# Performance work log

Measured on AMD Instinct MI355X. Metric: run time of the kernel, lower is better.

## Reference

```python
import jax, jax.numpy as jnp
import numpy as np

N = 50000      # nodes
E = 1600000    # edges
IN = 128       # in_channels
H = 64         # hidden_channels
P = 200000     # edge pairs to score
BN_EPS = 1e-5


def setup_inputs() -> dict:
    key = jax.random.key(0)
    ks = jax.random.split(key, 24)
    lin = lambda k, i, o: jax.random.normal(k, (i, o), jnp.float32) / np.sqrt(i).astype(np.float32)
    return {
        "x": jax.random.normal(ks[0], (N, IN), jnp.float32),
        "edge_index": jax.random.randint(ks[1], (2, E), 0, N, jnp.int32),
        "src": jax.random.randint(ks[2], (P,), 0, N, jnp.int32),
        "dst": jax.random.randint(ks[3], (P,), 0, N, jnp.int32),
        # GCNConv weights/biases
        "W1": lin(ks[4], IN, H),        "b1": jnp.zeros((H,), jnp.float32),
        "W2": lin(ks[5], H, 2 * H),     "b2": jnp.zeros((2 * H,), jnp.float32),
        "W3": lin(ks[6], 2 * H, 2 * H), "b3": jnp.zeros((2 * H,), jnp.float32),
        # BatchNorm affine params
        "g1": jnp.ones((H,), jnp.float32),     "bt1": jnp.zeros((H,), jnp.float32),
        "g2": jnp.ones((2 * H,), jnp.float32), "bt2": jnp.zeros((2 * H,), jnp.float32),
        "g3": jnp.ones((2 * H,), jnp.float32), "bt3": jnp.zeros((2 * H,), jnp.float32),
        # edge-scoring MLP: Linear(4H -> 2H), ReLU, Linear(2H -> 1)
        "fcW1": lin(ks[7], 4 * H, 2 * H), "fcb1": jnp.zeros((2 * H,), jnp.float32),
        "fcW2": lin(ks[8], 2 * H, 1),     "fcb2": jnp.zeros((1,), jnp.float32),
    }


def _gcn_norm(edge_index):
    # add self-loops, symmetric normalization D^-1/2 (A+I) D^-1/2
    loop = jnp.arange(N, dtype=edge_index.dtype)
    row = jnp.concatenate([edge_index[0], loop])
    col = jnp.concatenate([edge_index[1], loop])
    deg = jax.ops.segment_sum(jnp.ones(row.shape, jnp.float32), col, num_segments=N)
    dis = jnp.where(deg > 0, jax.lax.rsqrt(deg), 0.0)
    norm = dis[row] * dis[col]
    return row, col, norm


def _conv(x, W, b, row, col, norm):
    h = x @ W                                  # [N, C]
    msg = h[row] * norm[:, None]               # [E+N, C] gather + scale
    agg = jax.ops.segment_sum(msg, col, num_segments=N)
    return agg + b


def _bn(x, g, bt):
    mu = x.mean(0)
    var = x.var(0)
    return g * (x - mu) * jax.lax.rsqrt(var + BN_EPS) + bt


def reference(x, edge_index, src, dst,
              W1, b1, W2, b2, W3, b3,
              g1, bt1, g2, bt2, g3, bt3,
              fcW1, fcb1, fcW2, fcb2):
    row, col, norm = _gcn_norm(edge_index)
    # inference path: dropout is identity; BN uses batch statistics
    z = _bn(jax.nn.relu(_conv(x, W1, b1, row, col, norm)), g1, bt1)
    z = _bn(jax.nn.relu(_conv(z, W2, b2, row, col, norm)), g2, bt2)
    z = _bn(jax.nn.relu(_conv(z, W3, b3, row, col, norm)), g3, bt3)
    # score(): gather-concat-MLP over edge pairs
    emb = jnp.concatenate([z[src], z[dst]], axis=1)   # [P, 4H]
    hidden = jax.nn.relu(emb @ fcW1 + fcb1)
    scores = (hidden @ fcW2 + fcb2).squeeze(-1)       # [P]
    return scores
```

## Files before the change

### kernel.cpp

```cpp
#include <hip/hip_runtime.h>
#include <math.h>

typedef short bf16x8 __attribute__((ext_vector_type(8)));
typedef float f32x4 __attribute__((ext_vector_type(4)));

#define BCAP 17408

__device__ inline unsigned int f2bf_pack(float lo, float hi) {
    unsigned int ul = __builtin_bit_cast(unsigned int, lo);
    unsigned int uh = __builtin_bit_cast(unsigned int, hi);
    ul = ul + 0x7fffu + ((ul >> 16) & 1u);
    uh = uh + 0x7fffu + ((uh >> 16) & 1u);
    return (ul >> 16) | (uh & 0xffff0000u);
}
__device__ inline unsigned short f2bf(float f) {
    unsigned int u = __builtin_bit_cast(unsigned int, f);
    u = u + 0x7fffu + ((u >> 16) & 1u);
    return (unsigned short)(u >> 16);
}
__device__ inline float bf2f(unsigned short u) {
    return __builtin_bit_cast(float, (unsigned int)u << 16);
}
__device__ inline float bflo(unsigned int w) { return __builtin_bit_cast(float, w << 16); }
__device__ inline float bfhi(unsigned int w) { return __builtin_bit_cast(float, w & 0xffff0000u); }


__global__ void k_seed(int* bcur, int NB) {
    int b = threadIdx.x;
    if (b < NB) bcur[b] = b * BCAP;
}

__global__ __launch_bounds__(256) void k_binA(const int* __restrict__ row, const int* __restrict__ col,
                                              int* __restrict__ bcur, int2* __restrict__ binned,
                                              int E, int NB) {
    constexpr int SLOTS = 32;
    constexpr int CHUNK = 2048;
    __shared__ int2 stage[128][SLOTS];
    __shared__ int lcount[128];
    for (int b = threadIdx.x; b < 128; b += 256) lcount[b] = 0;
    __syncthreads();
    for (int cs = blockIdx.x * CHUNK; cs < E; cs += gridDim.x * CHUNK) {
#pragma unroll
        for (int j = 0; j < CHUNK / 256; ++j) {
            int e = cs + j * 256 + threadIdx.x;
            if (e < E) {
                int r = row[e], c = col[e];
                int b = c >> 9;
                int pos = atomicAdd(&lcount[b], 1);
                if (pos < SLOTS) stage[b][pos] = make_int2(r, c);
                else {
                    int gp = atomicAdd(&bcur[b], 1);
                    binned[gp] = make_int2(r, c);
                }
            }
        }
        __syncthreads();
        for (int b = threadIdx.x; b < NB; b += 256) {
            int c = lcount[b];
            if (c > SLOTS) c = SLOTS;
            if (c > 0) {
                int gp = atomicAdd(&bcur[b], c);
                for (int j = 0; j < c; ++j) binned[gp + j] = stage[b][j];
            }
            lcount[b] = 0;
        }
        __syncthreads();
    }
}

__global__ void k_btop(const int* __restrict__ bcur, int* __restrict__ bstart,
                       int* __restrict__ offs, int NB, int N) {
    if (threadIdx.x == 0) {
        int acc = 0;
        for (int b = 0; b < NB; b++) {
            bstart[b] = acc;
            acc += bcur[b] - b * BCAP;
        }
        bstart[NB] = acc;
        offs[N] = acc;
    }
}

__global__ __launch_bounds__(1024) void k_binB1(const int2* __restrict__ binned, const int* __restrict__ bcur,
                                                const int* __restrict__ bstart, int* __restrict__ offs,
                                                float* __restrict__ dis, int N) {
    __shared__ int cnt[512];
    const int b = blockIdx.x;
    const int lo = b << 9;
    const int slab = b * BCAP;
    const int count = bcur[b] - slab;
    if (threadIdx.x < 512) cnt[threadIdx.x] = 0;
    __syncthreads();
    for (int i = threadIdx.x; i < count; i += 1024)
        atomicAdd(&cnt[binned[slab + i].y - lo], 1);
    __syncthreads();
    int own = 0;
    if (threadIdx.x < 512) own = cnt[threadIdx.x];
    for (int off = 1; off < 512; off <<= 1) {
        int t = 0;
        if (threadIdx.x < 512 && threadIdx.x >= off) t = cnt[threadIdx.x - off];
        __syncthreads();
        if (threadIdx.x < 512) cnt[threadIdx.x] += t;
        __syncthreads();
    }
    if (threadIdx.x < 512 && lo + threadIdx.x < N) {
        offs[lo + threadIdx.x] = bstart[b] + cnt[threadIdx.x] - own;
        dis[lo + threadIdx.x] = 1.0f / sqrtf((float)(own + 1));
    }
}

__global__ __launch_bounds__(1024) void k_binB2(const int2* __restrict__ binned, const int* __restrict__ bcur,
                                                const int* __restrict__ bstart, const int* __restrict__ offs,
                                                const float* __restrict__ dis, int2* __restrict__ csr, int N) {
    __shared__ int2 stage[BCAP];
    __shared__ int cur[512];
    const int b = blockIdx.x;
    const int lo = b << 9;
    const int slab = b * BCAP;
    const int count = bcur[b] - slab;
    const int base = bstart[b];
    if (threadIdx.x < 512) {
        int node = lo + threadIdx.x;
        cur[threadIdx.x] = (node < N ? offs[node] : base + count) - base;
    }
    __syncthreads();
    for (int i = threadIdx.x; i < count; i += 1024) {
        int2 e = binned[slab + i];
        int slot = atomicAdd(&cur[e.y - lo], 1);
        int2 o = make_int2(e.x, __builtin_bit_cast(int, dis[e.x]));
        if (slot < BCAP) stage[slot] = o;
        else csr[base + slot] = o;
    }
    __syncthreads();
    int lim = count < BCAP ? count : BCAP;
    for (int i = threadIdx.x; i < lim; i += 1024) csr[base + i] = stage[i];
}


__global__ __launch_bounds__(256) void k_cast(const float* __restrict__ X, unsigned short* __restrict__ Y, int n8) {
    int i = blockIdx.x * 256 + threadIdx.x;
    if (i >= n8) return;
    const float4* x4 = (const float4*)X;
    float4 a = x4[2 * i], b = x4[2 * i + 1];
    uint4 o = make_uint4(f2bf_pack(a.x, a.y), f2bf_pack(a.z, a.w),
                         f2bf_pack(b.x, b.y), f2bf_pack(b.z, b.w));
    *(uint4*)(Y + (size_t)i * 8) = o;
}


template <int K, int COUT>
__global__ __launch_bounds__(256) void k_prep(const float* __restrict__ W, unsigned short* __restrict__ Wt) {
    constexpr int NG = (COUT / 16) * (K / 32) * 64;
    int g = blockIdx.x * 256 + threadIdx.x;
    if (g >= NG) return;
    int l = g & 63;
    int ks = (g >> 6) % (K / 32);
    int nt = g / (64 * (K / 32));
    int n = nt * 16 + (l & 15);
    int k0 = ks * 32 + (l >> 4) * 8;
    unsigned int w[4];
#pragma unroll
    for (int j = 0; j < 4; ++j) {
        float a = W[(size_t)(k0 + 2 * j) * COUT + n];
        float b = W[(size_t)(k0 + 2 * j + 1) * COUT + n];
        w[j] = f2bf_pack(a, b);
    }
    *(uint4*)(Wt + (size_t)g * 8) = make_uint4(w[0], w[1], w[2], w[3]);
}


template <int K, int COUT, bool FUSED>
__global__ __launch_bounds__(256) void k_mgemm(const unsigned short* __restrict__ Xb,
                                               const unsigned short* __restrict__ Wt,
                                               const float* __restrict__ bias,
                                               unsigned short* __restrict__ H,
                                               float* __restrict__ part, int n) {
    constexpr int NT = COUT / 16;
    constexpr int KS = K / 32;
    __shared__ float reds[FUSED ? 16 : 1][COUT];
    __shared__ float redq[FUSED ? 16 : 1][COUT];
    const int lane = threadIdx.x & 63;
    const int wave = threadIdx.x >> 6;
    const int m = lane & 15, g4 = lane >> 4;
    const int rb = blockIdx.x * 64 + wave * 16;

    bf16x8 af[KS];
    {
        int arow = rb + m;
        if (arow >= n) arow = n - 1;
        const unsigned short* xr = Xb + (size_t)arow * K + g4 * 8;
#pragma unroll
        for (int ks = 0; ks < KS; ++ks) af[ks] = *(const bf16x8*)(xr + ks * 32);
    }
    const bf16x8* Wv = (const bf16x8*)Wt;
    f32x4 acc[NT];
#pragma unroll
    for (int nt = 0; nt < NT; ++nt) {
        f32x4 a = {0.f, 0.f, 0.f, 0.f};
#pragma unroll
        for (int ks = 0; ks < KS; ++ks)
            a = __builtin_amdgcn_mfma_f32_16x16x32_bf16(af[ks], Wv[(nt * KS + ks) * 64 + lane], a, 0, 0, 0);
        acc[nt] = a;
    }

    if (!FUSED) {
#pragma unroll
        for (int nt = 0; nt < NT; ++nt)
#pragma unroll
            for (int r = 0; r < 4; ++r) {
                int gr = rb + g4 * 4 + r;
                if (gr < n) H[(size_t)gr * COUT + nt * 16 + m] = f2bf(acc[nt][r]);
            }
    } else {
        float vs[NT], vq[NT];
#pragma unroll
        for (int nt = 0; nt < NT; ++nt) {
            float b1 = bias[nt * 16 + m];
            vs[nt] = 0.f; vq[nt] = 0.f;
#pragma unroll
            for (int r = 0; r < 4; ++r) {
                int gr = rb + g4 * 4 + r;
                bool ok = gr < n;
                float val = ok ? fmaxf(acc[nt][r] + b1, 0.f) : 0.f;
                if (ok) H[(size_t)gr * COUT + nt * 16 + m] = f2bf(val);
                vs[nt] += val;
                vq[nt] += val * val;
            }
        }
#pragma unroll
        for (int nt = 0; nt < NT; ++nt) {
            reds[wave * 4 + g4][nt * 16 + m] = vs[nt];
            redq[wave * 4 + g4][nt * 16 + m] = vq[nt];
        }
        __syncthreads();
        for (int c = threadIdx.x; c < COUT; c += 256) {
            float S = 0.f, Q = 0.f;
#pragma unroll
            for (int t = 0; t < 16; ++t) { S += reds[t][c]; Q += redq[t][c]; }
            part[(size_t)blockIdx.x * 2 * COUT + c] = S;
            part[(size_t)blockIdx.x * 2 * COUT + COUT + c] = Q;
        }
    }
}


__global__ __launch_bounds__(256) void k_agg64(const unsigned short* __restrict__ H, const int* __restrict__ offs,
                                               const int2* __restrict__ csr, const float* __restrict__ dis,
                                               const float* __restrict__ bias, unsigned short* __restrict__ Y,
                                               float* __restrict__ part, int n) {
    const int lane = threadIdx.x & 63;
    const int wave = threadIdx.x >> 6;
    const int gw = blockIdx.x * 4 + wave;
    const int nw = gridDim.x * 4;
    float bsum = 0.f, bsq = 0.f;
    const float bias_r = bias[lane];

    for (int node = gw; node < n; node += nw) {
        int s0 = offs[node], s1 = offs[node + 1];
        float a = 0.f;
        int e = s0;
        for (; e + 4 <= s1; e += 4) {
            int2 e0 = csr[e], e1 = csr[e + 1], e2 = csr[e + 2], e3 = csr[e + 3];
            float h0 = bf2f(H[(size_t)e0.x * 64 + lane]);
            float h1 = bf2f(H[(size_t)e1.x * 64 + lane]);
            float h2 = bf2f(H[(size_t)e2.x * 64 + lane]);
            float h3 = bf2f(H[(size_t)e3.x * 64 + lane]);
            a += __builtin_bit_cast(float, e0.y) * h0 + __builtin_bit_cast(float, e1.y) * h1;
            a += __builtin_bit_cast(float, e2.y) * h2 + __builtin_bit_cast(float, e3.y) * h3;
        }
        for (; e < s1; ++e) {
            int2 e0 = csr[e];
            a += __builtin_bit_cast(float, e0.y) * bf2f(H[(size_t)e0.x * 64 + lane]);
        }
        float dn = dis[node];
        float val = a * dn + bf2f(H[(size_t)node * 64 + lane]) * dn * dn + bias_r;
        val = fmaxf(val, 0.f);
        Y[(size_t)node * 64 + lane] = f2bf(val);
        bsum += val;
        bsq += val * val;
    }
    __shared__ float psum[4][64], psq[4][64];
    psum[wave][lane] = bsum; psq[wave][lane] = bsq;
    __syncthreads();
    if (threadIdx.x < 64) {
        int c = threadIdx.x;
        float s = psum[0][c] + psum[1][c] + psum[2][c] + psum[3][c];
        float qq = psq[0][c] + psq[1][c] + psq[2][c] + psq[3][c];
        part[(size_t)blockIdx.x * 128 + c] = s;
        part[(size_t)blockIdx.x * 128 + 64 + c] = qq;
    }
}


template <int C>
__global__ __launch_bounds__(256) void k_aggpre(const unsigned short* __restrict__ IN, const int* __restrict__ offs,
                                                const int2* __restrict__ csr, const float* __restrict__ dis,
                                                const float* __restrict__ ss, unsigned short* __restrict__ OUT, int n) {
    constexpr int VPL = C / 64;
    const int lane = threadIdx.x & 63;
    const int wave = threadIdx.x >> 6;
    const int gw = blockIdx.x * 4 + wave;
    const int nw = gridDim.x * 4;
    float sc[VPL], sh[VPL];
#pragma unroll
    for (int q = 0; q < VPL; q++) { sc[q] = ss[lane * VPL + q]; sh[q] = ss[C + lane * VPL + q]; }

    for (int node = gw; node < n; node += nw) {
        int s0 = offs[node], s1 = offs[node + 1];
        float a[VPL];
        float S = 0.f;
#pragma unroll
        for (int q = 0; q < VPL; q++) a[q] = 0.f;
        int e = s0;
        for (; e + 4 <= s1; e += 4) {
            int2 e0 = csr[e], e1 = csr[e + 1], e2 = csr[e + 2], e3 = csr[e + 3];
            float v0 = __builtin_bit_cast(float, e0.y);
            float v1 = __builtin_bit_cast(float, e1.y);
            float v2 = __builtin_bit_cast(float, e2.y);
            float v3 = __builtin_bit_cast(float, e3.y);
            S += (v0 + v1) + (v2 + v3);
            if (VPL == 2) {
                unsigned int w0 = *(const unsigned int*)(IN + (size_t)e0.x * C + 2 * lane);
                unsigned int w1 = *(const unsigned int*)(IN + (size_t)e1.x * C + 2 * lane);
                unsigned int w2 = *(const unsigned int*)(IN + (size_t)e2.x * C + 2 * lane);
                unsigned int w3 = *(const unsigned int*)(IN + (size_t)e3.x * C + 2 * lane);
                a[0] += v0 * bflo(w0) + v1 * bflo(w1) + v2 * bflo(w2) + v3 * bflo(w3);
                a[1] += v0 * bfhi(w0) + v1 * bfhi(w1) + v2 * bfhi(w2) + v3 * bfhi(w3);
            } else {
                float h0 = bf2f(IN[(size_t)e0.x * C + lane]);
                float h1 = bf2f(IN[(size_t)e1.x * C + lane]);
                float h2 = bf2f(IN[(size_t)e2.x * C + lane]);
                float h3 = bf2f(IN[(size_t)e3.x * C + lane]);
                a[0] += v0 * h0 + v1 * h1 + v2 * h2 + v3 * h3;
            }
        }
        for (; e < s1; ++e) {
            int2 e0 = csr[e];
            float v0 = __builtin_bit_cast(float, e0.y);
            S += v0;
            if (VPL == 2) {
                unsigned int w0 = *(const unsigned int*)(IN + (size_t)e0.x * C + 2 * lane);
                a[0] += v0 * bflo(w0);
                a[1] += v0 * bfhi(w0);
            } else {
                a[0] += v0 * bf2f(IN[(size_t)e0.x * C + lane]);
            }
        }
        float dn = dis[node];
        float shf = S + dn;
        if (VPL == 2) {
            unsigned int wsf = *(const unsigned int*)(IN + (size_t)node * C + 2 * lane);
            float o0 = dn * ((a[0] + dn * bflo(wsf)) * sc[0] + shf * sh[0]);
            float o1 = dn * ((a[1] + dn * bfhi(wsf)) * sc[1] + shf * sh[1]);
            *(unsigned int*)(OUT + (size_t)node * C + 2 * lane) = f2bf_pack(o0, o1);
        } else {
            float hsf = bf2f(IN[(size_t)node * C + lane]);
            OUT[(size_t)node * C + lane] = f2bf(dn * ((a[0] + dn * hsf) * sc[0] + shf * sh[0]));
        }
    }
}


template <int C>
__global__ __launch_bounds__(1024) void k_bnfin(const float* __restrict__ part, int nblk,
                                                const float* __restrict__ g, const float* __restrict__ bt,
                                                float* __restrict__ ss, int n) {
    constexpr int ROWS = 1024 / C;
    __shared__ float ssum[1024], ssq[1024];
    const int c = threadIdx.x % C;
    const int r = threadIdx.x / C;
    float s = 0.f, q = 0.f;
    for (int b = r; b < nblk; b += ROWS) {
        s += part[(size_t)b * 2 * C + c];
        q += part[(size_t)b * 2 * C + C + c];
    }
    ssum[threadIdx.x] = s; ssq[threadIdx.x] = q;
    __syncthreads();
    if (r == 0) {
        double S = (double)s, Q = (double)q;
        for (int rr = 1; rr < ROWS; rr++) { S += (double)ssum[rr * C + c]; Q += (double)ssq[rr * C + c]; }
        double invN = 1.0 / (double)n;
        double mu = S * invN;
        double var = Q * invN - mu * mu;
        float scale = g[c] / sqrtf((float)var + 1e-5f);
        ss[c] = scale;
        ss[C + c] = bt[c] - (float)mu * scale;
    }
}


__global__ __launch_bounds__(128) void k_score(const unsigned short* __restrict__ Z, const float* __restrict__ ss,
                                               const int* __restrict__ src, const int* __restrict__ dst,
                                               const unsigned short* __restrict__ Wt,
                                               const float* __restrict__ fcb1, const float* __restrict__ fcW2,
                                               const float* __restrict__ fcb2, float* __restrict__ out, int P) {
    __shared__ unsigned int emb[2][16][128];
    const int lane = threadIdx.x & 63;
    const int wave = threadIdx.x >> 6;
    unsigned int (*Ew)[128] = emb[wave];
    const int tile = blockIdx.x * 2 + wave;
    const int pbase = tile * 16;

    const float2 sc2 = *(const float2*)&ss[2 * lane];
    const float2 sh2 = *(const float2*)&ss[128 + 2 * lane];

#pragma unroll 4
    for (int p = 0; p < 16; ++p) {
        int pi = pbase + p;
        int is = src[pi], id = dst[pi];
        unsigned int wa = *(const unsigned int*)(Z + (size_t)is * 128 + 2 * lane);
        unsigned int wb = *(const unsigned int*)(Z + (size_t)id * 128 + 2 * lane);
        unsigned int ua = f2bf_pack(bflo(wa) * sc2.x + sh2.x, bfhi(wa) * sc2.y + sh2.y);
        unsigned int ub = f2bf_pack(bflo(wb) * sc2.x + sh2.x, bfhi(wb) * sc2.y + sh2.y);
        int swz = (p & 7) << 4;
        char* rowp = (char*)&Ew[p][0];
        *(unsigned int*)(rowp + ((lane * 4) ^ swz)) = ua;
        *(unsigned int*)(rowp + (((lane + 64) * 4) ^ swz)) = ub;
    }

    const int m = lane & 15;
    const int g4 = lane >> 4;
    bf16x8 af[8];
    {
        const char* rowp = (const char*)&Ew[m][0];
        const int sw = (m & 7) << 4;
#pragma unroll
        for (int ks = 0; ks < 8; ++ks)
            af[ks] = *(const bf16x8*)(rowp + ((ks * 64 + g4 * 16) ^ sw));
    }

    float sacc[4] = {0.f, 0.f, 0.f, 0.f};
    const bf16x8* Wtv = (const bf16x8*)Wt;
#pragma unroll 2
    for (int nt = 0; nt < 8; ++nt) {
        f32x4 acc = {0.f, 0.f, 0.f, 0.f};
#pragma unroll
        for (int ks = 0; ks < 8; ++ks) {
            bf16x8 bf = Wtv[(nt * 8 + ks) * 64 + lane];
            acc = __builtin_amdgcn_mfma_f32_16x16x32_bf16(af[ks], bf, acc, 0, 0, 0);
        }
        int oc = nt * 16 + m;
        float b1 = fcb1[oc];
        float w2 = fcW2[oc];
#pragma unroll
        for (int r = 0; r < 4; ++r) {
            float h = fmaxf(acc[r] + b1, 0.f);
            sacc[r] += h * w2;
        }
    }

    const float b2v = fcb2[0];
#pragma unroll
    for (int r = 0; r < 4; ++r) {
        float s = sacc[r];
        s += __shfl_xor(s, 1);
        s += __shfl_xor(s, 2);
        s += __shfl_xor(s, 4);
        s += __shfl_xor(s, 8);
        if (m == 0) out[pbase + g4 * 4 + r] = s + b2v;
    }
}


extern "C" void kernel_launch(void* const* d_in, const int* in_sizes, int n_in,
                              void* d_out, int out_size, void* d_ws, size_t ws_size,
                              hipStream_t stream) {
    const float* x   = (const float*)d_in[0];
    const int* ei    = (const int*)d_in[1];
    const int* src   = (const int*)d_in[2];
    const int* dst   = (const int*)d_in[3];
    const float* W1  = (const float*)d_in[4];
    const float* b1  = (const float*)d_in[5];
    const float* W2  = (const float*)d_in[6];
    const float* b2  = (const float*)d_in[7];
    const float* W3  = (const float*)d_in[8];
    const float* b3  = (const float*)d_in[9];
    const float* g1  = (const float*)d_in[10];
    const float* bt1 = (const float*)d_in[11];
    const float* g2  = (const float*)d_in[12];
    const float* bt2 = (const float*)d_in[13];
    const float* g3  = (const float*)d_in[14];
    const float* bt3 = (const float*)d_in[15];
    const float* fcW1 = (const float*)d_in[16];
    const float* fcb1 = (const float*)d_in[17];
    const float* fcW2 = (const float*)d_in[18];
    const float* fcb2 = (const float*)d_in[19];
    float* out = (float*)d_out;

    const int N = in_sizes[0] / 128;
    const int E = in_sizes[1] / 2;
    const int P = in_sizes[2];
    const int* erow = ei;
    const int* ecol = ei + E;
    const int NB = (N + 511) >> 9;

    const int AGG_GRID = 2048;

    char* w = (char*)d_ws;
    auto alloc = [&](size_t bytes) { void* p = (void*)w; w += (bytes + 255) & ~(size_t)255; return p; };
    float* dis     = (float*)alloc((size_t)N * 4);
    int*   offs    = (int*)alloc((size_t)(N + 1) * 4);
    int*   bcur    = (int*)alloc((size_t)128 * 4);
    int*   bstart  = (int*)alloc((size_t)(NB + 1) * 4);
    int2*  csr     = (int2*)alloc((size_t)E * 8);
    int2*  binned  = (int2*)alloc((size_t)NB * BCAP * 8);
    float* part    = (float*)alloc((size_t)AGG_GRID * 256 * 4);
    float* ss1     = (float*)alloc(2 * 64 * 4);
    float* ss2     = (float*)alloc(2 * 128 * 4);
    float* ss3     = (float*)alloc(2 * 128 * 4);
    unsigned short* Wts = (unsigned short*)alloc((size_t)4096 * 8 * 2);
    unsigned short* Wt1 = (unsigned short*)alloc((size_t)1024 * 8 * 2);
    unsigned short* Wt2 = (unsigned short*)alloc((size_t)1024 * 8 * 2);
    unsigned short* Wt3 = (unsigned short*)alloc((size_t)2048 * 8 * 2);
    unsigned short* Xb1 = (unsigned short*)alloc((size_t)N * 128 * 2);
    unsigned short* bhA = (unsigned short*)alloc((size_t)N * 128 * 2);
    unsigned short* bhB = (unsigned short*)alloc((size_t)N * 128 * 2);
    (void)ws_size; (void)n_in; (void)out_size;

    k_seed<<<1, 128, 0, stream>>>(bcur, NB);
    k_binA<<<256, 256, 0, stream>>>(erow, ecol, bcur, binned, E, NB);
    k_btop<<<1, 64, 0, stream>>>(bcur, bstart, offs, NB, N);
    k_binB1<<<NB, 1024, 0, stream>>>(binned, bcur, bstart, offs, dis, N);
    k_binB2<<<NB, 1024, 0, stream>>>(binned, bcur, bstart, offs, dis, csr, N);

    k_prep<256, 128><<<16, 256, 0, stream>>>(fcW1, Wts);
    k_prep<128, 64><<<4, 256, 0, stream>>>(W1, Wt1);
    k_prep<64, 128><<<4, 256, 0, stream>>>(W2, Wt2);
    k_prep<128, 128><<<8, 256, 0, stream>>>(W3, Wt3);
    k_cast<<<(N * 16 + 255) / 256, 256, 0, stream>>>(x, Xb1, N * 16);

    const int gemm_grid = (N + 63) / 64;

    k_mgemm<128, 64, false><<<gemm_grid, 256, 0, stream>>>(Xb1, Wt1, nullptr, bhA, nullptr, N);
    k_agg64<<<AGG_GRID, 256, 0, stream>>>(bhA, offs, csr, dis, b1, bhB, part, N);
    k_bnfin<64><<<1, 1024, 0, stream>>>(part, AGG_GRID, g1, bt1, ss1, N);

    k_aggpre<64><<<AGG_GRID, 256, 0, stream>>>(bhB, offs, csr, dis, ss1, Xb1, N);
    k_mgemm<64, 128, true><<<gemm_grid, 256, 0, stream>>>(Xb1, Wt2, b2, bhA, part, N);
    k_bnfin<128><<<1, 1024, 0, stream>>>(part, gemm_grid, g2, bt2, ss2, N);

    k_aggpre<128><<<AGG_GRID, 256, 0, stream>>>(bhA, offs, csr, dis, ss2, Xb1, N);
    k_mgemm<128, 128, true><<<gemm_grid, 256, 0, stream>>>(Xb1, Wt3, b3, bhB, part, N);
    k_bnfin<128><<<1, 1024, 0, stream>>>(part, gemm_grid, g3, bt3, ss3, N);

    const int score_grid = P / 32;
    k_score<<<score_grid, 128, 0, stream>>>(bhB, ss3, src, dst, Wts, fcb1, fcW2, fcb2, out, P);
}
```

Measured before the change: 511.4 us.

## Pack CSR edges into 32-bit words and fuse setup kernels

Edges are packed as 16-bit row and 16-bit column in binning, and CSR entries become 32-bit words holding a 16-bit source index plus a bf16 normalization weight, halving edge traffic in binning and all three aggregation passes. The seed, cast and weight-prep kernels are merged into one launch, and the bucket prefix scan is folded into binB1, which removes several small launches. This relies on N fitting in 16 bits (N=50000 fits) and lowers the precision of the edge weights to bf16.

```diff
diff --git a/kernel.cpp b/kernel.cpp
--- a/kernel.cpp
+++ b/kernel.cpp
@@ -25,17 +25,61 @@
 __device__ inline float bfhi(unsigned int w) { return __builtin_bit_cast(float, w & 0xffff0000u); }
 
 
-__global__ void k_seed(int* bcur, int NB) {
-    int b = threadIdx.x;
-    if (b < NB) bcur[b] = b * BCAP;
-}
+template <int K, int COUT>
+__device__ inline void prep_body(const float* __restrict__ W, unsigned short* __restrict__ Wt, int blk) {
+    constexpr int NG = (COUT / 16) * (K / 32) * 64;
+    int g = blk * 256 + threadIdx.x;
+    if (g >= NG) return;
+    int l = g & 63;
+    int ks = (g >> 6) % (K / 32);
+    int nt = g / (64 * (K / 32));
+    int n = nt * 16 + (l & 15);
+    int k0 = ks * 32 + (l >> 4) * 8;
+    unsigned int w[4];
+#pragma unroll
+    for (int j = 0; j < 4; ++j) {
+        float a = W[(size_t)(k0 + 2 * j) * COUT + n];
+        float b = W[(size_t)(k0 + 2 * j + 1) * COUT + n];
+        w[j] = f2bf_pack(a, b);
+    }
+    *(uint4*)(Wt + (size_t)g * 8) = make_uint4(w[0], w[1], w[2], w[3]);
+}
+
+__global__ __launch_bounds__(256) void k_prepall(const float* __restrict__ x, const float* __restrict__ fcW1,
+                                                 const float* __restrict__ W1, const float* __restrict__ W2,
+                                                 const float* __restrict__ W3,
+                                                 unsigned short* __restrict__ Xb1, unsigned short* __restrict__ Wts,
+                                                 unsigned short* __restrict__ Wt1, unsigned short* __restrict__ Wt2,
+                                                 unsigned short* __restrict__ Wt3, int* __restrict__ bcur,
+                                                 int n8, int NB) {
+    const int castBlocks = (n8 + 255) >> 8;
+    int b = blockIdx.x;
+    if (b < castBlocks) {
+        int i = b * 256 + threadIdx.x;
+        if (i < n8) {
+            const float4* x4 = (const float4*)x;
+            float4 a = x4[2 * i], c = x4[2 * i + 1];
+            uint4 o = make_uint4(f2bf_pack(a.x, a.y), f2bf_pack(a.z, a.w),
+                                 f2bf_pack(c.x, c.y), f2bf_pack(c.z, c.w));
+            *(uint4*)(Xb1 + (size_t)i * 8) = o;
+        }
+        return;
+    }
+    int rb = b - castBlocks;
+    if (rb < 16)      prep_body<256, 128>(fcW1, Wts, rb);
+    else if (rb < 20) prep_body<128, 64>(W1, Wt1, rb - 16);
+    else if (rb < 24) prep_body<64, 128>(W2, Wt2, rb - 20);
+    else if (rb < 32) prep_body<128, 128>(W3, Wt3, rb - 24);
+    else { if (threadIdx.x < NB) bcur[threadIdx.x] = threadIdx.x * BCAP; }
+}
+
 
 __global__ __launch_bounds__(256) void k_binA(const int* __restrict__ row, const int* __restrict__ col,
-                                              int* __restrict__ bcur, int2* __restrict__ binned,
+                                              int* __restrict__ bcur, unsigned int* __restrict__ binned,
                                               int E, int NB) {
     constexpr int SLOTS = 32;
     constexpr int CHUNK = 2048;
-    __shared__ int2 stage[128][SLOTS];
+    __shared__ unsigned int stage[128][SLOTS];
     __shared__ int lcount[128];
     for (int b = threadIdx.x; b < 128; b += 256) lcount[b] = 0;
     __syncthreads();
@@ -44,13 +88,14 @@
         for (int j = 0; j < CHUNK / 256; ++j) {
             int e = cs + j * 256 + threadIdx.x;
             if (e < E) {
-                int r = row[e], c = col[e];
+                unsigned int r = (unsigned int)row[e], c = (unsigned int)col[e];
+                unsigned int packed = (r << 16) | c;
                 int b = c >> 9;
                 int pos = atomicAdd(&lcount[b], 1);
-                if (pos < SLOTS) stage[b][pos] = make_int2(r, c);
+                if (pos < SLOTS) stage[b][pos] = packed;
                 else {
                     int gp = atomicAdd(&bcur[b], 1);
-                    binned[gp] = make_int2(r, c);
+                    binned[gp] = packed;
                 }
             }
         }
@@ -68,31 +113,27 @@
     }
 }
 
-__global__ void k_btop(const int* __restrict__ bcur, int* __restrict__ bstart,
-                       int* __restrict__ offs, int NB, int N) {
-    if (threadIdx.x == 0) {
-        int acc = 0;
-        for (int b = 0; b < NB; b++) {
-            bstart[b] = acc;
-            acc += bcur[b] - b * BCAP;
-        }
-        bstart[NB] = acc;
-        offs[N] = acc;
-    }
-}
-
-__global__ __launch_bounds__(1024) void k_binB1(const int2* __restrict__ binned, const int* __restrict__ bcur,
-                                                const int* __restrict__ bstart, int* __restrict__ offs,
-                                                float* __restrict__ dis, int N) {
+__global__ __launch_bounds__(1024) void k_binB1(const unsigned int* __restrict__ binned, const int* __restrict__ bcur,
+                                                int* __restrict__ offs, float* __restrict__ dis, int N, int NB) {
     __shared__ int cnt[512];
+    __shared__ int bpre[129];
     const int b = blockIdx.x;
     const int lo = b << 9;
     const int slab = b * BCAP;
     const int count = bcur[b] - slab;
     if (threadIdx.x < 512) cnt[threadIdx.x] = 0;
-    __syncthreads();
+    if (threadIdx.x < NB) bpre[threadIdx.x] = bcur[threadIdx.x] - threadIdx.x * BCAP;
+    __syncthreads();
+    if (threadIdx.x == 0) {
+        int acc = 0;
+        for (int j = 0; j < NB; j++) { int t = bpre[j]; bpre[j] = acc; acc += t; }
+        bpre[NB] = acc;
+        if (b == 0) offs[N] = acc;
+    }
+    __syncthreads();
+    const int base = bpre[b];
     for (int i = threadIdx.x; i < count; i += 1024)
-        atomicAdd(&cnt[binned[slab + i].y - lo], 1);
+        atomicAdd(&cnt[(binned[slab + i] & 0xffffu) - lo], 1);
     __syncthreads();
     int own = 0;
     if (threadIdx.x < 512) own = cnt[threadIdx.x];
@@ -104,68 +145,38 @@
         __syncthreads();
     }
     if (threadIdx.x < 512 && lo + threadIdx.x < N) {
-        offs[lo + threadIdx.x] = bstart[b] + cnt[threadIdx.x] - own;
+        offs[lo + threadIdx.x] = base + cnt[threadIdx.x] - own;
         dis[lo + threadIdx.x] = 1.0f / sqrtf((float)(own + 1));
     }
 }
 
-__global__ __launch_bounds__(1024) void k_binB2(const int2* __restrict__ binned, const int* __restrict__ bcur,
-                                                const int* __restrict__ bstart, const int* __restrict__ offs,
-                                                const float* __restrict__ dis, int2* __restrict__ csr, int N) {
-    __shared__ int2 stage[BCAP];
+__global__ __launch_bounds__(1024) void k_binB2(const unsigned int* __restrict__ binned, const int* __restrict__ bcur,
+                                                const int* __restrict__ offs, const float* __restrict__ dis,
+                                                unsigned int* __restrict__ csr, int N) {
+    __shared__ unsigned int stage[BCAP];
     __shared__ int cur[512];
     const int b = blockIdx.x;
     const int lo = b << 9;
     const int slab = b * BCAP;
     const int count = bcur[b] - slab;
-    const int base = bstart[b];
+    const int base = offs[lo];
     if (threadIdx.x < 512) {
         int node = lo + threadIdx.x;
         cur[threadIdx.x] = (node < N ? offs[node] : base + count) - base;
     }
     __syncthreads();
     for (int i = threadIdx.x; i < count; i += 1024) {
-        int2 e = binned[slab + i];
-        int slot = atomicAdd(&cur[e.y - lo], 1);
-        int2 o = make_int2(e.x, __builtin_bit_cast(int, dis[e.x]));
+        unsigned int e = binned[slab + i];
+        unsigned int c = e & 0xffffu;
+        unsigned int r = e >> 16;
+        int slot = atomicAdd(&cur[c - lo], 1);
+        unsigned int o = r | ((unsigned int)f2bf(dis[r]) << 16);
         if (slot < BCAP) stage[slot] = o;
         else csr[base + slot] = o;
     }
     __syncthreads();
     int lim = count < BCAP ? count : BCAP;
     for (int i = threadIdx.x; i < lim; i += 1024) csr[base + i] = stage[i];
-}
-
-
-__global__ __launch_bounds__(256) void k_cast(const float* __restrict__ X, unsigned short* __restrict__ Y, int n8) {
-    int i = blockIdx.x * 256 + threadIdx.x;
-    if (i >= n8) return;
-    const float4* x4 = (const float4*)X;
-    float4 a = x4[2 * i], b = x4[2 * i + 1];
-    uint4 o = make_uint4(f2bf_pack(a.x, a.y), f2bf_pack(a.z, a.w),
-                         f2bf_pack(b.x, b.y), f2bf_pack(b.z, b.w));
-    *(uint4*)(Y + (size_t)i * 8) = o;
-}
-
-
-template <int K, int COUT>
-__global__ __launch_bounds__(256) void k_prep(const float* __restrict__ W, unsigned short* __restrict__ Wt) {
-    constexpr int NG = (COUT / 16) * (K / 32) * 64;
-    int g = blockIdx.x * 256 + threadIdx.x;
-    if (g >= NG) return;
-    int l = g & 63;
-    int ks = (g >> 6) % (K / 32);
-    int nt = g / (64 * (K / 32));
-    int n = nt * 16 + (l & 15);
-    int k0 = ks * 32 + (l >> 4) * 8;
-    unsigned int w[4];
-#pragma unroll
-    for (int j = 0; j < 4; ++j) {
-        float a = W[(size_t)(k0 + 2 * j) * COUT + n];
-        float b = W[(size_t)(k0 + 2 * j + 1) * COUT + n];
-        w[j] = f2bf_pack(a, b);
-    }
-    *(uint4*)(Wt + (size_t)g * 8) = make_uint4(w[0], w[1], w[2], w[3]);
 }
 
 
@@ -245,7 +256,7 @@
 
 
 __global__ __launch_bounds__(256) void k_agg64(const unsigned short* __restrict__ H, const int* __restrict__ offs,
-                                               const int2* __restrict__ csr, const float* __restrict__ dis,
+                                               const unsigned int* __restrict__ csr, const float* __restrict__ dis,
                                                const float* __restrict__ bias, unsigned short* __restrict__ Y,
                                                float* __restrict__ part, int n) {
     const int lane = threadIdx.x & 63;
@@ -260,17 +271,17 @@
         float a = 0.f;
         int e = s0;
         for (; e + 4 <= s1; e += 4) {
-            int2 e0 = csr[e], e1 = csr[e + 1], e2 = csr[e + 2], e3 = csr[e + 3];
-            float h0 = bf2f(H[(size_t)e0.x * 64 + lane]);
-            float h1 = bf2f(H[(size_t)e1.x * 64 + lane]);
-            float h2 = bf2f(H[(size_t)e2.x * 64 + lane]);
-            float h3 = bf2f(H[(size_t)e3.x * 64 + lane]);
-            a += __builtin_bit_cast(float, e0.y) * h0 + __builtin_bit_cast(float, e1.y) * h1;
-            a += __builtin_bit_cast(float, e2.y) * h2 + __builtin_bit_cast(float, e3.y) * h3;
+            unsigned int e0 = csr[e], e1 = csr[e + 1], e2 = csr[e + 2], e3 = csr[e + 3];
+            float h0 = bf2f(H[(size_t)(e0 & 0xffffu) * 64 + lane]);
+            float h1 = bf2f(H[(size_t)(e1 & 0xffffu) * 64 + lane]);
+            float h2 = bf2f(H[(size_t)(e2 & 0xffffu) * 64 + lane]);
+            float h3 = bf2f(H[(size_t)(e3 & 0xffffu) * 64 + lane]);
+            a += bfhi(e0) * h0 + bfhi(e1) * h1;
+            a += bfhi(e2) * h2 + bfhi(e3) * h3;
         }
         for (; e < s1; ++e) {
-            int2 e0 = csr[e];
-            a += __builtin_bit_cast(float, e0.y) * bf2f(H[(size_t)e0.x * 64 + lane]);
+            unsigned int e0 = csr[e];
+            a += bfhi(e0) * bf2f(H[(size_t)(e0 & 0xffffu) * 64 + lane]);
         }
         float dn = dis[node];
         float val = a * dn + bf2f(H[(size_t)node * 64 + lane]) * dn * dn + bias_r;
@@ -294,7 +305,7 @@
 
 template <int C>
 __global__ __launch_bounds__(256) void k_aggpre(const unsigned short* __restrict__ IN, const int* __restrict__ offs,
-                                                const int2* __restrict__ csr, const float* __restrict__ dis,
+                                                const unsigned int* __restrict__ csr, const float* __restrict__ dis,
                                                 const float* __restrict__ ss, unsigned short* __restrict__ OUT, int n) {
     constexpr int VPL = C / 64;
     const int lane = threadIdx.x & 63;
@@ -313,37 +324,34 @@
         for (int q = 0; q < VPL; q++) a[q] = 0.f;
         int e = s0;
         for (; e + 4 <= s1; e += 4) {
-            int2 e0 = csr[e], e1 = csr[e + 1], e2 = csr[e + 2], e3 = csr[e + 3];
-            float v0 = __builtin_bit_cast(float, e0.y);
-            float v1 = __builtin_bit_cast(float, e1.y);
-            float v2 = __builtin_bit_cast(float, e2.y);
-            float v3 = __builtin_bit_cast(float, e3.y);
+            unsigned int e0 = csr[e], e1 = csr[e + 1], e2 = csr[e + 2], e3 = csr[e + 3];
+            float v0 = bfhi(e0), v1 = bfhi(e1), v2 = bfhi(e2), v3 = bfhi(e3);
             S += (v0 + v1) + (v2 + v3);
             if (VPL == 2) {
-                unsigned int w0 = *(const unsigned int*)(IN + (size_t)e0.x * C + 2 * lane);
-                unsigned int w1 = *(const unsigned int*)(IN + (size_t)e1.x * C + 2 * lane);
-                unsigned int w2 = *(const unsigned int*)(IN + (size_t)e2.x * C + 2 * lane);
-                unsigned int w3 = *(const unsigned int*)(IN + (size_t)e3.x * C + 2 * lane);
+                unsigned int w0 = *(const unsigned int*)(IN + (size_t)(e0 & 0xffffu) * C + 2 * lane);
+                unsigned int w1 = *(const unsigned int*)(IN + (size_t)(e1 & 0xffffu) * C + 2 * lane);
+                unsigned int w2 = *(const unsigned int*)(IN + (size_t)(e2 & 0xffffu) * C + 2 * lane);
+                unsigned int w3 = *(const unsigned int*)(IN + (size_t)(e3 & 0xffffu) * C + 2 * lane);
                 a[0] += v0 * bflo(w0) + v1 * bflo(w1) + v2 * bflo(w2) + v3 * bflo(w3);
                 a[1] += v0 * bfhi(w0) + v1 * bfhi(w1) + v2 * bfhi(w2) + v3 * bfhi(w3);
             } else {
-                float h0 = bf2f(IN[(size_t)e0.x * C + lane]);
-                float h1 = bf2f(IN[(size_t)e1.x * C + lane]);
-                float h2 = bf2f(IN[(size_t)e2.x * C + lane]);
-                float h3 = bf2f(IN[(size_t)e3.x * C + lane]);
+                float h0 = bf2f(IN[(size_t)(e0 & 0xffffu) * C + lane]);
+                float h1 = bf2f(IN[(size_t)(e1 & 0xffffu) * C + lane]);
+                float h2 = bf2f(IN[(size_t)(e2 & 0xffffu) * C + lane]);
+                float h3 = bf2f(IN[(size_t)(e3 & 0xffffu) * C + lane]);
                 a[0] += v0 * h0 + v1 * h1 + v2 * h2 + v3 * h3;
             }
         }
         for (; e < s1; ++e) {
-            int2 e0 = csr[e];
-            float v0 = __builtin_bit_cast(float, e0.y);
+            unsigned int e0 = csr[e];
+            float v0 = bfhi(e0);
             S += v0;
             if (VPL == 2) {
-                unsigned int w0 = *(const unsigned int*)(IN + (size_t)e0.x * C + 2 * lane);
+                unsigned int w0 = *(const unsigned int*)(IN + (size_t)(e0 & 0xffffu) * C + 2 * lane);
                 a[0] += v0 * bflo(w0);
                 a[1] += v0 * bfhi(w0);
             } else {
-                a[0] += v0 * bf2f(IN[(size_t)e0.x * C + lane]);
+                a[0] += v0 * bf2f(IN[(size_t)(e0 & 0xffffu) * C + lane]);
             }
         }
         float dn = dis[node];
@@ -501,9 +509,8 @@
     float* dis     = (float*)alloc((size_t)N * 4);
     int*   offs    = (int*)alloc((size_t)(N + 1) * 4);
     int*   bcur    = (int*)alloc((size_t)128 * 4);
-    int*   bstart  = (int*)alloc((size_t)(NB + 1) * 4);
-    int2*  csr     = (int2*)alloc((size_t)E * 8);
-    int2*  binned  = (int2*)alloc((size_t)NB * BCAP * 8);
+    unsigned int* csr    = (unsigned int*)alloc((size_t)E * 4);
+    unsigned int* binned = (unsigned int*)alloc((size_t)NB * BCAP * 4);
     float* part    = (float*)alloc((size_t)AGG_GRID * 256 * 4);
     float* ss1     = (float*)alloc(2 * 64 * 4);
     float* ss2     = (float*)alloc(2 * 128 * 4);
@@ -517,17 +524,13 @@
     unsigned short* bhB = (unsigned short*)alloc((size_t)N * 128 * 2);
     (void)ws_size; (void)n_in; (void)out_size;
 
-    k_seed<<<1, 128, 0, stream>>>(bcur, NB);
+    const int n8 = N * 16;
+    const int castBlocks = (n8 + 255) >> 8;
+    k_prepall<<<castBlocks + 33, 256, 0, stream>>>(x, fcW1, W1, W2, W3, Xb1, Wts, Wt1, Wt2, Wt3, bcur, n8, NB);
+
     k_binA<<<256, 256, 0, stream>>>(erow, ecol, bcur, binned, E, NB);
-    k_btop<<<1, 64, 0, stream>>>(bcur, bstart, offs, NB, N);
-    k_binB1<<<NB, 1024, 0, stream>>>(binned, bcur, bstart, offs, dis, N);
-    k_binB2<<<NB, 1024, 0, stream>>>(binned, bcur, bstart, offs, dis, csr, N);
-
-    k_prep<256, 128><<<16, 256, 0, stream>>>(fcW1, Wts);
-    k_prep<128, 64><<<4, 256, 0, stream>>>(W1, Wt1);
-    k_prep<64, 128><<<4, 256, 0, stream>>>(W2, Wt2);
-    k_prep<128, 128><<<8, 256, 0, stream>>>(W3, Wt3);
-    k_cast<<<(N * 16 + 255) / 256, 256, 0, stream>>>(x, Xb1, N * 16);
+    k_binB1<<<NB, 1024, 0, stream>>>(binned, bcur, offs, dis, N, NB);
+    k_binB2<<<NB, 1024, 0, stream>>>(binned, bcur, offs, dis, csr, N);
 
     const int gemm_grid = (N + 63) / 64;
 
```

After: 488.2 us. 1.05x faster.
